# Optimization experiments

Hardware: AMD Instinct MI355X
Metric: run time of the kernel (lower is better)

Reference implementation:

```python
import jax, jax.numpy as jnp
import numpy as np

RES = 64  # hardcoded in Mapping_2.maps_to_kp_2
EPS = 1e-6


def setup_inputs() -> dict:
    key = jax.random.key(0)
    k1, k2, k3, k4, k5 = jax.random.split(key, 5)
    B = 256
    return {
        "front_vec": jax.random.normal(k1, (B, 40, RES, RES), dtype=jnp.float32),
        "front_dis": jax.random.uniform(k2, (B, 20, RES, RES), dtype=jnp.float32),
        "back_vec": jax.random.normal(k3, (B, 40, RES, RES), dtype=jnp.float32),
        "back_dis": jax.random.uniform(k4, (B, 20, RES, RES), dtype=jnp.float32),
        "ske_mask": jax.random.uniform(k5, (B, 20, RES, RES), dtype=jnp.float32),
    }


def reference(front_vec, front_dis, back_vec, back_dis, ske_mask):
    B = front_vec.shape[0]
    res = RES
    # Same row-major reshapes as torch .reshape
    fv = front_vec.reshape(B, 20, res, res, 2)
    fd = front_dis.reshape(B, 20, res, res, 1)
    bv = back_vec.reshape(B, 20, res, res, 2)
    bd = back_dis.reshape(B, 20, res, res, 1)
    m = ske_mask.reshape(B, 20, res, res, 1)

    # locs[d0, d1] = (d0, d1), matching locs[:, i, y] = (i, y) in the torch code
    ar = jnp.arange(res, dtype=jnp.float32)
    locs = jnp.stack(jnp.meshgrid(ar, ar, indexing="ij"), axis=-1)  # [res,res,2]

    msum = jnp.sum(m, axis=(2, 3, 4))            # [B,20]
    denom = (msum + EPS)[..., None]              # [B,20,1]

    # Masked weighted-sum votes, normalized by mask mass: [B,20,2]
    F_ = jnp.sum(m * (fv * fd * res + locs), axis=(2, 3)) / denom
    Bk = jnp.sum(m * (bv * bd * res + locs), axis=(2, 3)) / denom

    # Root keypoint: average over the 5 finger-base channels (4*i), guarded by sum(mask)!=0
    root_terms = jnp.where((msum[:, ::4] != 0)[..., None], Bk[:, ::4], 0.0)  # [B,5,2]
    kp0 = jnp.sum(root_terms, axis=1) / 5.0       # [B,2]

    # Finger joints: kp[4i+4-j] = (F[4i+j] + Bk[4i+j+1])/2 for j<3, F[4i+3] for j=3
    Fg = F_.reshape(B, 5, 4, 2)
    Bg = Bk.reshape(B, 5, 4, 2)
    tail = jnp.stack(
        [
            Fg[:, :, 3],                          # kp[4i+1]
            (Fg[:, :, 2] + Bg[:, :, 3]) * 0.5,    # kp[4i+2]
            (Fg[:, :, 1] + Bg[:, :, 2]) * 0.5,    # kp[4i+3]
            (Fg[:, :, 0] + Bg[:, :, 1]) * 0.5,    # kp[4i+4]
        ],
        axis=2,
    )  # [B,5,4,2]

    kp = jnp.concatenate([kp0[:, None], tail.reshape(B, 20, 2)], axis=1)  # [B,21,2]
    return kp * 4.0
```

## Files before the change

### kernel.cpp

```cpp
#include <hip/hip_runtime.h>

#define RES 64
#define EPS 1e-6f

__global__ __launch_bounds__(256) void reduce_bk_kernel(
    const float* __restrict__ front_vec,
    const float* __restrict__ front_dis,
    const float* __restrict__ back_vec,
    const float* __restrict__ back_dis,
    const float* __restrict__ ske_mask,
    float* __restrict__ ws)
{
    const int bk = blockIdx.x;
    const int b  = bk / 20;
    const int k  = bk - b * 20;
    const int t  = threadIdx.x;

    const size_t base_v = (size_t)b * (40 * 4096) + (size_t)k * 8192;
    const size_t base_d = (size_t)b * (20 * 4096) + (size_t)k * 4096;

    const float4* __restrict__ fv4 = (const float4*)(front_vec + base_v);
    const float4* __restrict__ bv4 = (const float4*)(back_vec  + base_v);
    const float2* __restrict__ fd2 = (const float2*)(front_dis + base_d);
    const float2* __restrict__ bd2 = (const float2*)(back_dis  + base_d);
    const float2* __restrict__ m2  = (const float2*)(ske_mask  + base_d);

    float s_m = 0.f, s_F0 = 0.f, s_F1 = 0.f, s_B0 = 0.f, s_B1 = 0.f;

    #pragma unroll
    for (int it = 0; it < 8; ++it) {
        const int g  = it * 256 + t;
        const int p0 = g * 2;
        const float y  = (float)(p0 >> 6);
        const float x0 = (float)(p0 & 63);

        const float2 mv = m2[g];
        const float2 fd = fd2[g];
        const float2 bd = bd2[g];
        const float4 fv = fv4[g];
        const float4 bv = bv4[g];

        s_m += mv.x + mv.y;

        s_F0 += mv.x * fmaf(fv.x * fd.x, 64.f, y)
              + mv.y * fmaf(fv.z * fd.y, 64.f, y);
        s_F1 += mv.x * fmaf(fv.y * fd.x, 64.f, x0)
              + mv.y * fmaf(fv.w * fd.y, 64.f, x0 + 1.f);
        s_B0 += mv.x * fmaf(bv.x * bd.x, 64.f, y)
              + mv.y * fmaf(bv.z * bd.y, 64.f, y);
        s_B1 += mv.x * fmaf(bv.y * bd.x, 64.f, x0)
              + mv.y * fmaf(bv.w * bd.y, 64.f, x0 + 1.f);
    }

    #pragma unroll
    for (int off = 32; off > 0; off >>= 1) {
        s_m  += __shfl_down(s_m,  off);
        s_F0 += __shfl_down(s_F0, off);
        s_F1 += __shfl_down(s_F1, off);
        s_B0 += __shfl_down(s_B0, off);
        s_B1 += __shfl_down(s_B1, off);
    }

    __shared__ float red[4][5];
    const int wave = t >> 6;
    const int lane = t & 63;
    if (lane == 0) {
        red[wave][0] = s_m;
        red[wave][1] = s_F0;
        red[wave][2] = s_F1;
        red[wave][3] = s_B0;
        red[wave][4] = s_B1;
    }
    __syncthreads();
    if (t == 0) {
        float m = 0.f, F0 = 0.f, F1 = 0.f, B0 = 0.f, B1 = 0.f;
        #pragma unroll
        for (int w = 0; w < 4; ++w) {
            m  += red[w][0];
            F0 += red[w][1];
            F1 += red[w][2];
            B0 += red[w][3];
            B1 += red[w][4];
        }
        const float denom = m + EPS;
        float* o = ws + (size_t)bk * 8;
        o[0] = F0 / denom;
        o[1] = F1 / denom;
        o[2] = B0 / denom;
        o[3] = B1 / denom;
        o[4] = m;
    }
}

__global__ __launch_bounds__(256) void assemble_kernel(
    const float* __restrict__ ws, float* __restrict__ out, int B)
{
    const int b = blockIdx.x * blockDim.x + threadIdx.x;
    if (b >= B) return;

    float F[20][2], Bk[20][2], ms[20];
    #pragma unroll
    for (int k = 0; k < 20; ++k) {
        const float* w = ws + (size_t)(b * 20 + k) * 8;
        F[k][0]  = w[0];
        F[k][1]  = w[1];
        Bk[k][0] = w[2];
        Bk[k][1] = w[3];
        ms[k]    = w[4];
    }

    float r0 = 0.f, r1 = 0.f;
    #pragma unroll
    for (int i = 0; i < 5; ++i) {
        const int c = 4 * i;
        if (ms[c] != 0.f) { r0 += Bk[c][0]; r1 += Bk[c][1]; }
    }

    float* o = out + (size_t)b * 42;
    o[0] = (r0 / 5.f) * 4.f;
    o[1] = (r1 / 5.f) * 4.f;

    #pragma unroll
    for (int i = 0; i < 5; ++i) {
        const int c = 4 * i;
        float* p = o + 2 * (1 + 4 * i);
        p[0] = F[c + 3][0] * 4.f;
        p[1] = F[c + 3][1] * 4.f;
        p[2] = (F[c + 2][0] + Bk[c + 3][0]) * 2.f;
        p[3] = (F[c + 2][1] + Bk[c + 3][1]) * 2.f;
        p[4] = (F[c + 1][0] + Bk[c + 2][0]) * 2.f;
        p[5] = (F[c + 1][1] + Bk[c + 2][1]) * 2.f;
        p[6] = (F[c + 0][0] + Bk[c + 1][0]) * 2.f;
        p[7] = (F[c + 0][1] + Bk[c + 1][1]) * 2.f;
    }
}

extern "C" void kernel_launch(void* const* d_in, const int* in_sizes, int n_in,
                              void* d_out, int out_size, void* d_ws, size_t ws_size,
                              hipStream_t stream) {
    const float* front_vec = (const float*)d_in[0];
    const float* front_dis = (const float*)d_in[1];
    const float* back_vec  = (const float*)d_in[2];
    const float* back_dis  = (const float*)d_in[3];
    const float* ske_mask  = (const float*)d_in[4];
    float* out = (float*)d_out;
    float* ws  = (float*)d_ws;

    const int B = in_sizes[1] / (20 * RES * RES);
    const int nBK = B * 20;

    reduce_bk_kernel<<<nBK, 256, 0, stream>>>(
        front_vec, front_dis, back_vec, back_dis, ske_mask, ws);

    assemble_kernel<<<(B + 255) / 256, 256, 0, stream>>>(ws, out, B);
}
```

Baseline: 107.3 us.

## Fuse reduction and assembly into one kernel with one block per batch

Replaces the two-kernel pipeline (per-channel reduction blocks writing to a workspace, then an assembly kernel) with a single kernel launching one 640-thread block per batch item. Each wave reduces two channels and the block finishes the keypoint assembly in shared memory. This removes a kernel launch and the workspace round trip. In exchange the grid shrinks from B*20 blocks to B blocks with 10 waves each, and each wave walks two channels serially, which changes memory-level parallelism on a bandwidth-bound workload.

```diff
diff --git a/kernel.cpp b/kernel.cpp
--- a/kernel.cpp
+++ b/kernel.cpp
@@ -3,135 +3,118 @@
 #define RES 64
 #define EPS 1e-6f
 
-__global__ __launch_bounds__(256) void reduce_bk_kernel(
+__global__ __launch_bounds__(640) void fused_kernel(
     const float* __restrict__ front_vec,
     const float* __restrict__ front_dis,
     const float* __restrict__ back_vec,
     const float* __restrict__ back_dis,
     const float* __restrict__ ske_mask,
-    float* __restrict__ ws)
+    float* __restrict__ out)
 {
-    const int bk = blockIdx.x;
-    const int b  = bk / 20;
-    const int k  = bk - b * 20;
-    const int t  = threadIdx.x;
+    const int b    = blockIdx.x;
+    const int t    = threadIdx.x;
+    const int w    = t >> 6;
+    const int lane = t & 63;
 
-    const size_t base_v = (size_t)b * (40 * 4096) + (size_t)k * 8192;
-    const size_t base_d = (size_t)b * (20 * 4096) + (size_t)k * 4096;
-
-    const float4* __restrict__ fv4 = (const float4*)(front_vec + base_v);
-    const float4* __restrict__ bv4 = (const float4*)(back_vec  + base_v);
-    const float2* __restrict__ fd2 = (const float2*)(front_dis + base_d);
-    const float2* __restrict__ bd2 = (const float2*)(back_dis  + base_d);
-    const float2* __restrict__ m2  = (const float2*)(ske_mask  + base_d);
-
-    float s_m = 0.f, s_F0 = 0.f, s_F1 = 0.f, s_B0 = 0.f, s_B1 = 0.f;
+    __shared__ float red[20][5];
+    __shared__ float Fl[20][2], Bl[20][2], msl[20];
 
     #pragma unroll
-    for (int it = 0; it < 8; ++it) {
-        const int g  = it * 256 + t;
-        const int p0 = g * 2;
-        const float y  = (float)(p0 >> 6);
-        const float x0 = (float)(p0 & 63);
+    for (int cc = 0; cc < 2; ++cc) {
+        const int k = w * 2 + cc;
 
-        const float2 mv = m2[g];
-        const float2 fd = fd2[g];
-        const float2 bd = bd2[g];
-        const float4 fv = fv4[g];
-        const float4 bv = bv4[g];
+        const size_t base_v = (size_t)b * (40 * 4096) + (size_t)k * 8192;
+        const size_t base_d = (size_t)b * (20 * 4096) + (size_t)k * 4096;
 
-        s_m += mv.x + mv.y;
+        const float4* __restrict__ fv4 = (const float4*)(front_vec + base_v);
+        const float4* __restrict__ bv4 = (const float4*)(back_vec  + base_v);
+        const float2* __restrict__ fd2 = (const float2*)(front_dis + base_d);
+        const float2* __restrict__ bd2 = (const float2*)(back_dis  + base_d);
+        const float2* __restrict__ m2  = (const float2*)(ske_mask  + base_d);
 
-        s_F0 += mv.x * fmaf(fv.x * fd.x, 64.f, y)
-              + mv.y * fmaf(fv.z * fd.y, 64.f, y);
-        s_F1 += mv.x * fmaf(fv.y * fd.x, 64.f, x0)
-              + mv.y * fmaf(fv.w * fd.y, 64.f, x0 + 1.f);
-        s_B0 += mv.x * fmaf(bv.x * bd.x, 64.f, y)
-              + mv.y * fmaf(bv.z * bd.y, 64.f, y);
-        s_B1 += mv.x * fmaf(bv.y * bd.x, 64.f, x0)
-              + mv.y * fmaf(bv.w * bd.y, 64.f, x0 + 1.f);
+        float s_m = 0.f, s_F0 = 0.f, s_F1 = 0.f, s_B0 = 0.f, s_B1 = 0.f;
+
+        #pragma unroll 4
+        for (int i = 0; i < 32; ++i) {
+            const int g  = i * 64 + lane;
+            const int p0 = g * 2;
+            const float y  = (float)(p0 >> 6);
+            const float x0 = (float)(p0 & 63);
+
+            const float2 mv = m2[g];
+            const float2 fd = fd2[g];
+            const float2 bd = bd2[g];
+            const float4 fv = fv4[g];
+            const float4 bv = bv4[g];
+
+            s_m += mv.x + mv.y;
+
+            s_F0 += mv.x * fmaf(fv.x * fd.x, 64.f, y)
+                  + mv.y * fmaf(fv.z * fd.y, 64.f, y);
+            s_F1 += mv.x * fmaf(fv.y * fd.x, 64.f, x0)
+                  + mv.y * fmaf(fv.w * fd.y, 64.f, x0 + 1.f);
+            s_B0 += mv.x * fmaf(bv.x * bd.x, 64.f, y)
+                  + mv.y * fmaf(bv.z * bd.y, 64.f, y);
+            s_B1 += mv.x * fmaf(bv.y * bd.x, 64.f, x0)
+                  + mv.y * fmaf(bv.w * bd.y, 64.f, x0 + 1.f);
+        }
+
+        #pragma unroll
+        for (int off = 32; off > 0; off >>= 1) {
+            s_m  += __shfl_down(s_m,  off);
+            s_F0 += __shfl_down(s_F0, off);
+            s_F1 += __shfl_down(s_F1, off);
+            s_B0 += __shfl_down(s_B0, off);
+            s_B1 += __shfl_down(s_B1, off);
+        }
+
+        if (lane == 0) {
+            red[k][0] = s_m;
+            red[k][1] = s_F0;
+            red[k][2] = s_F1;
+            red[k][3] = s_B0;
+            red[k][4] = s_B1;
+        }
     }
 
-    #pragma unroll
-    for (int off = 32; off > 0; off >>= 1) {
-        s_m  += __shfl_down(s_m,  off);
-        s_F0 += __shfl_down(s_F0, off);
-        s_F1 += __shfl_down(s_F1, off);
-        s_B0 += __shfl_down(s_B0, off);
-        s_B1 += __shfl_down(s_B1, off);
-    }
+    __syncthreads();
 
-    __shared__ float red[4][5];
-    const int wave = t >> 6;
-    const int lane = t & 63;
-    if (lane == 0) {
-        red[wave][0] = s_m;
-        red[wave][1] = s_F0;
-        red[wave][2] = s_F1;
-        red[wave][3] = s_B0;
-        red[wave][4] = s_B1;
+    if (t < 20) {
+        const float m     = red[t][0];
+        const float denom = m + EPS;
+        Fl[t][0] = red[t][1] / denom;
+        Fl[t][1] = red[t][2] / denom;
+        Bl[t][0] = red[t][3] / denom;
+        Bl[t][1] = red[t][4] / denom;
+        msl[t]   = m;
     }
     __syncthreads();
+
     if (t == 0) {
-        float m = 0.f, F0 = 0.f, F1 = 0.f, B0 = 0.f, B1 = 0.f;
+        float r0 = 0.f, r1 = 0.f;
         #pragma unroll
-        for (int w = 0; w < 4; ++w) {
-            m  += red[w][0];
-            F0 += red[w][1];
-            F1 += red[w][2];
-            B0 += red[w][3];
-            B1 += red[w][4];
+        for (int i = 0; i < 5; ++i) {
+            const int c = 4 * i;
+            if (msl[c] != 0.f) { r0 += Bl[c][0]; r1 += Bl[c][1]; }
         }
-        const float denom = m + EPS;
-        float* o = ws + (size_t)bk * 8;
-        o[0] = F0 / denom;
-        o[1] = F1 / denom;
-        o[2] = B0 / denom;
-        o[3] = B1 / denom;
-        o[4] = m;
-    }
-}
 
-__global__ __launch_bounds__(256) void assemble_kernel(
-    const float* __restrict__ ws, float* __restrict__ out, int B)
-{
-    const int b = blockIdx.x * blockDim.x + threadIdx.x;
-    if (b >= B) return;
+        float* o = out + (size_t)b * 42;
+        o[0] = (r0 / 5.f) * 4.f;
+        o[1] = (r1 / 5.f) * 4.f;
 
-    float F[20][2], Bk[20][2], ms[20];
-    #pragma unroll
-    for (int k = 0; k < 20; ++k) {
-        const float* w = ws + (size_t)(b * 20 + k) * 8;
-        F[k][0]  = w[0];
-        F[k][1]  = w[1];
-        Bk[k][0] = w[2];
-        Bk[k][1] = w[3];
-        ms[k]    = w[4];
-    }
-
-    float r0 = 0.f, r1 = 0.f;
-    #pragma unroll
-    for (int i = 0; i < 5; ++i) {
-        const int c = 4 * i;
-        if (ms[c] != 0.f) { r0 += Bk[c][0]; r1 += Bk[c][1]; }
-    }
-
-    float* o = out + (size_t)b * 42;
-    o[0] = (r0 / 5.f) * 4.f;
-    o[1] = (r1 / 5.f) * 4.f;
-
-    #pragma unroll
-    for (int i = 0; i < 5; ++i) {
-        const int c = 4 * i;
-        float* p = o + 2 * (1 + 4 * i);
-        p[0] = F[c + 3][0] * 4.f;
-        p[1] = F[c + 3][1] * 4.f;
-        p[2] = (F[c + 2][0] + Bk[c + 3][0]) * 2.f;
-        p[3] = (F[c + 2][1] + Bk[c + 3][1]) * 2.f;
-        p[4] = (F[c + 1][0] + Bk[c + 2][0]) * 2.f;
-        p[5] = (F[c + 1][1] + Bk[c + 2][1]) * 2.f;
-        p[6] = (F[c + 0][0] + Bk[c + 1][0]) * 2.f;
-        p[7] = (F[c + 0][1] + Bk[c + 1][1]) * 2.f;
+        #pragma unroll
+        for (int i = 0; i < 5; ++i) {
+            const int c = 4 * i;
+            float* p = o + 2 * (1 + 4 * i);
+            p[0] = Fl[c + 3][0] * 4.f;
+            p[1] = Fl[c + 3][1] * 4.f;
+            p[2] = (Fl[c + 2][0] + Bl[c + 3][0]) * 2.f;
+            p[3] = (Fl[c + 2][1] + Bl[c + 3][1]) * 2.f;
+            p[4] = (Fl[c + 1][0] + Bl[c + 2][0]) * 2.f;
+            p[5] = (Fl[c + 1][1] + Bl[c + 2][1]) * 2.f;
+            p[6] = (Fl[c + 0][0] + Bl[c + 1][0]) * 2.f;
+            p[7] = (Fl[c + 0][1] + Bl[c + 1][1]) * 2.f;
+        }
     }
 }
 
@@ -144,13 +127,9 @@
     const float* back_dis  = (const float*)d_in[3];
     const float* ske_mask  = (const float*)d_in[4];
     float* out = (float*)d_out;
-    float* ws  = (float*)d_ws;
 
     const int B = in_sizes[1] / (20 * RES * RES);
-    const int nBK = B * 20;
 
-    reduce_bk_kernel<<<nBK, 256, 0, stream>>>(
-        front_vec, front_dis, back_vec, back_dis, ske_mask, ws);
-
-    assemble_kernel<<<(B + 255) / 256, 256, 0, stream>>>(ws, out, B);
+    fused_kernel<<<B, 640, 0, stream>>>(
+        front_vec, front_dis, back_vec, back_dis, ske_mask, out);
 }
```

Result: faster. 102.0 us (-5.0%).
